# Kernel optimization log

Measured on AMD Instinct MI355X. Metric: run time of the kernel, lower is better.

Reference implementation:

```python
import jax, jax.numpy as jnp
import numpy as np

B, C, P, H, W = 8, 256, 64, 64, 64


def conv2d(x, w, b, pad):
    y = jax.lax.conv_general_dilated(
        x, w, window_strides=(1, 1), padding=[(pad, pad), (pad, pad)],
        dimension_numbers=("NCHW", "OIHW", "NCHW"))
    return y + b[None, :, None, None]


def setup_inputs() -> dict:
    key = jax.random.key(0)
    ks = jax.random.split(key, 9)
    x = jax.random.normal(ks[0], (B, C, H, W), dtype=jnp.float32)
    # conv weights, OIHW layout; scale ~ kaiming-ish
    w_top = jax.random.normal(ks[1], (P, C, 1, 1), jnp.float32) * (1.0 / np.sqrt(C))
    b_top = jnp.zeros((P,), jnp.float32)
    w_center = jax.random.normal(ks[2], (P, C, 1, 1), jnp.float32) * (1.0 / np.sqrt(C))
    b_center = jnp.zeros((P,), jnp.float32)
    w_bottom = jax.random.normal(ks[3], (C, C, 3, 3), jnp.float32) * (1.0 / np.sqrt(9 * C))
    b_bottom = jnp.zeros((C,), jnp.float32)
    w_out = jax.random.normal(ks[4], (C, C, 3, 3), jnp.float32) * (1.0 / np.sqrt(9 * C))
    b_out = jnp.zeros((C,), jnp.float32)
    return {"x": x, "w_top": w_top, "b_top": b_top, "w_center": w_center,
            "b_center": b_center, "w_bottom": w_bottom, "b_bottom": b_bottom,
            "w_out": w_out, "b_out": b_out}


def reference(x, w_top, b_top, w_center, b_center, w_bottom, b_bottom, w_out, b_out):
    b, c, h, w = x.shape
    hw = h * w
    x_top = conv2d(x, w_top, b_top, 0).reshape(b, -1, hw)          # [B, P, HW]
    x_center = conv2d(x, w_center, b_center, 0).reshape(b, -1, hw)  # [B, P, HW]
    x_center = jnp.swapaxes(x_center, 1, 2)                          # [B, HW, P]
    x_bottom = conv2d(x, w_bottom, b_bottom, 1).reshape(b, c, hw)
    x_bottom = jnp.swapaxes(x_bottom, 1, 2)                          # [B, HW, C]
    sp_map = jnp.einsum("bnp,bpm->bnm", x_center, x_top)            # [B, HW, HW]
    # NOTE: softmax is GLOBAL over the flattened HW*HW map per batch element,
    # not per-row (faithful to original Softmax(dim=1) on view(bsize, -1)).
    sp_map = jax.nn.softmax(sp_map.reshape(b, -1), axis=1).reshape(b, hw, hw)
    sp_map = jnp.einsum("bnm,bmc->bnc", sp_map, x_bottom)           # [B, HW, C]
    # NOTE: original does .reshape(b, C, h, w) on a [B, HW, C] tensor (no
    # transpose) -- replicate that exact memory reinterpretation.
    sp_map = sp_map.reshape(b, c, h, w)
    return conv2d(x + sp_map, w_out, b_out, 1)
```

## Files before the change

### kernel.cpp

```cpp
#include <hip/hip_runtime.h>
#include <hip/hip_bf16.h>
#include <type_traits>

constexpr int B_ = 8, C_ = 256, P_ = 64, H_ = 64, W_ = 64, HW_ = 4096;

typedef __attribute__((ext_vector_type(8))) short short8;
typedef __attribute__((ext_vector_type(4))) short short4v;
typedef __attribute__((ext_vector_type(4))) float f32x4;

__device__ __forceinline__ short bfbits(float f) {
    __hip_bfloat16 h = __float2bfloat16(f);
    return *reinterpret_cast<short*>(&h);
}
__device__ __forceinline__ float bf2f(short s) {
    __hip_bfloat16 h = *reinterpret_cast<__hip_bfloat16*>(&s);
    return (float)h;
}

#define GLL16(gsrc, ldst)                                                      \
    __builtin_amdgcn_global_load_lds(                                         \
        (const __attribute__((address_space(1))) void*)(gsrc),                \
        (__attribute__((address_space(3))) void*)(ldst), 16, 0, 0)


__global__ __launch_bounds__(256) void k_prep_w(
    const float* __restrict__ w, short8* __restrict__ wbP)
{
    const int idx = blockIdx.x * 256 + threadIdx.x;
    const int lane = idx & 63, cot = (idx >> 6) & 15;
    const int cb = (idx >> 10) & 7, tap = idx >> 13;
    const int lm = lane & 15, lq = lane >> 4;
    const int co = cot * 16 + lm, ci0 = cb * 32 + lq * 8;
    short8 v;
#pragma unroll
    for (int k = 0; k < 8; ++k)
        v[k] = bfbits(w[(co * 256 + ci0 + k) * 9 + tap]);
    wbP[idx] = v;
}

__global__ __launch_bounds__(256) void k_pack_xb(
    const __hip_bfloat16* __restrict__ xb, short8* __restrict__ xbP)
{
    const int tid = blockIdx.x * 256 + threadIdx.x;
    const int lane = tid & 63, wid = tid >> 6;
    const int ct = wid & 15, g = (wid >> 4) & 127, b = wid >> 11;
    const int c = ct * 16 + (lane >> 2);
    const int mo = g * 32 + (lane & 3) * 8;
    const short8 v = *reinterpret_cast<const short8*>(
        &xb[((size_t)(b * 256 + c)) * HW_ + mo]);
    xbP[(size_t)wid * 64 + (lane & 3) * 16 + (lane >> 2)] = v;
}

__global__ __launch_bounds__(256) void k_conv1x1(
    const float* __restrict__ x,
    const float* __restrict__ w_top, const float* __restrict__ b_top,
    const float* __restrict__ w_cen, const float* __restrict__ b_cen,
    short8* __restrict__ xtPh, short8* __restrict__ xtPl,
    short8* __restrict__ xcPh, short8* __restrict__ xcPl)
{
    const int b = blockIdx.z;
    const int n = blockIdx.x * 256 + threadIdx.x;
    const int conv = blockIdx.y >> 2, pq = blockIdx.y & 3;
    const int p0 = pq * 16;
    const float* w    = conv ? w_cen : w_top;
    const float* bias = conv ? b_cen : b_top;
    short8* oh = conv ? xcPh : xtPh;
    short8* ol = conv ? xcPl : xtPl;

    const float* xp = x + (size_t)b * C_ * HW_ + n;
    float acc[16];
#pragma unroll
    for (int p = 0; p < 16; ++p) acc[p] = 0.f;

    for (int c = 0; c < C_; c += 4) {
        const float xv0 = xp[(size_t)(c + 0) * HW_];
        const float xv1 = xp[(size_t)(c + 1) * HW_];
        const float xv2 = xp[(size_t)(c + 2) * HW_];
        const float xv3 = xp[(size_t)(c + 3) * HW_];
#pragma unroll
        for (int p = 0; p < 16; ++p) {
            const float4 wv = *reinterpret_cast<const float4*>(&w[(p0 + p) * C_ + c]);
            float a = acc[p];
            a = fmaf(wv.x, xv0, a);
            a = fmaf(wv.y, xv1, a);
            a = fmaf(wv.z, xv2, a);
            a = fmaf(wv.w, xv3, a);
            acc[p] = a;
        }
    }
    const int nt = n >> 4, lmn = n & 15;
    const size_t obase = ((size_t)(b * 256 + nt) * 2 + (pq >> 1)) * 64 + lmn;
#pragma unroll
    for (int jj = 0; jj < 2; ++jj) {
        short8 vh, vl;
#pragma unroll
        for (int k = 0; k < 8; ++k) {
            const float v = acc[jj * 8 + k] + bias[p0 + jj * 8 + k];
            const short hb = bfbits(v);
            vh[k] = hb;
            vl[k] = bfbits(v - bf2f(hb));
        }
        const size_t idx = obase + (size_t)(((pq & 1) * 2 + jj) * 16);
        oh[idx] = vh;
        ol[idx] = vl;
    }
}

template <typename OT>
__global__ __launch_bounds__(512, 4) void k_conv3x3_mfma(
    const float* __restrict__ xin, const short8* __restrict__ wbP,
    const float* __restrict__ bias, OT* __restrict__ out)
{
    __shared__ __align__(16) __hip_bfloat16 Xs[3][66][40];
    const int lin = blockIdx.x;
    const int b = lin & 7, h = lin >> 3;
    const int t = threadIdx.x;
    const int wave = t >> 6, lane = t & 63;
    const int lm = lane & 15, lq = lane >> 4;
    const int cobase = wave * 32;
    const int cot0 = wave * 2;

    f32x4 acc[4][2];
#pragma unroll
    for (int i = 0; i < 4; ++i)
#pragma unroll
        for (int j = 0; j < 2; ++j) acc[i][j] = f32x4{0.f, 0.f, 0.f, 0.f};

    if (t < 192) {
        const int r = t >> 6, cc = t & 31, side = (t >> 5) & 1;
        Xs[r][side ? 65 : 0][cc] = __float2bfloat16(0.f);
    }

    const float* xbase = xin + (size_t)b * C_ * HW_;

    for (int cb = 0; cb < 8; ++cb) {
        const int ci0 = cb * 32;
        __syncthreads();
#pragma unroll
        for (int it = 0; it < 3; ++it) {
            const int idx = it * 512 + t;
            const int r = idx >> 9, ci = (idx >> 4) & 31, wq = idx & 15;
            const int hh = h + r - 1;
            float4 v = {0.f, 0.f, 0.f, 0.f};
            if (hh >= 0 && hh < H_)
                v = *reinterpret_cast<const float4*>(
                    &xbase[(size_t)(ci0 + ci) * HW_ + hh * W_ + wq * 4]);
            Xs[r][1 + wq * 4 + 0][ci] = __float2bfloat16(v.x);
            Xs[r][1 + wq * 4 + 1][ci] = __float2bfloat16(v.y);
            Xs[r][1 + wq * 4 + 2][ci] = __float2bfloat16(v.z);
            Xs[r][1 + wq * 4 + 3][ci] = __float2bfloat16(v.w);
        }
        __syncthreads();

#pragma unroll 3
        for (int tap = 0; tap < 9; ++tap) {
            const int dh = tap / 3;
            const int dw = tap % 3;
            const short8* wp = wbP + ((size_t)(tap * 8 + cb)) * 1024 + lane;
            short8 af[2];
            af[0] = wp[(cot0 + 0) * 64];
            af[1] = wp[(cot0 + 1) * 64];
            short8 bf[4];
#pragma unroll
            for (int nt = 0; nt < 4; ++nt)
                bf[nt] = *reinterpret_cast<const short8*>(
                    &Xs[dh][nt * 16 + lm + dw][lq * 8]);
#pragma unroll
            for (int nt = 0; nt < 4; ++nt)
#pragma unroll
                for (int ct = 0; ct < 2; ++ct)
                    acc[nt][ct] = __builtin_amdgcn_mfma_f32_16x16x32_bf16(
                        af[ct], bf[nt], acc[nt][ct], 0, 0, 0);
        }
    }

#pragma unroll
    for (int nt = 0; nt < 4; ++nt) {
        const int pos = h * W_ + nt * 16 + lm;
#pragma unroll
        for (int ct = 0; ct < 2; ++ct) {
            const int co = cobase + ct * 16 + lq * 4;
#pragma unroll
            for (int r = 0; r < 4; ++r) {
                const float v = acc[nt][ct][r] + bias[co + r];
                if constexpr (std::is_same<OT, __hip_bfloat16>::value)
                    out[((size_t)(b * C_ + co + r)) * HW_ + pos] = __float2bfloat16(v);
                else
                    out[((size_t)(b * C_ + co + r)) * HW_ + pos] = v;
            }
        }
    }
}

__global__ __launch_bounds__(512, 2) void k_attn_mfma(
    const short8* __restrict__ xtPh, const short8* __restrict__ xtPl,
    const short8* __restrict__ xcPh, const short8* __restrict__ xcPl,
    const short8* __restrict__ xbP, float* __restrict__ O,
    float* __restrict__ Z)
{
    extern __shared__ __align__(16) char smem[];
    short8* XTs = (short8*)smem;
    short8* XBs = (short8*)(smem + 32768);
    short8* Ps8 = (short8*)(smem + 98304);
    short4v* Ps4 = (short4v*)(smem + 98304);
    float* zred = (float*)(smem + 114688);

    const int lin = blockIdx.x;
    const int b = lin & 7, nblk = lin >> 3;
    const int n0 = nblk * 128;

    const int t = threadIdx.x, wv = t >> 6, lane = t & 63;
    const int lm = lane & 15, lq = lane >> 4;
    const int mh = wv >> 2, nq2 = wv & 3;
    const int nq = wv >> 2, cq = wv & 3;

    short8 cB2[2][2][2];
#pragma unroll
    for (int ntile = 0; ntile < 2; ++ntile) {
        const int gt = nblk * 8 + nq2 * 2 + ntile;
        const size_t base = ((size_t)(b * 256 + gt) * 2) * 64 + lane;
        cB2[ntile][0][0] = xcPh[base];
        cB2[ntile][1][0] = xcPh[base + 64];
        cB2[ntile][0][1] = xcPl[base];
        cB2[ntile][1][1] = xcPl[base + 64];
    }
    asm volatile("s_waitcnt vmcnt(0)" ::: "memory");

    auto stage = [&](int smt, int bufi) {
        short8* XT = XTs + bufi * 1024;
        short8* XB = XBs + bufi * 2048;
        const size_t abase = ((size_t)(b * 512 + smt * 8)) * 64;
#pragma unroll
        for (int k = 0; k < 2; ++k) {
            const int c = wv * 2 + k, ms = c >> 2, part = c & 3;
            const short8* src = (part < 2 ? xtPh : xtPl)
                                + abase + ms * 128 + (part & 1) * 64 + lane;
            GLL16(src, XT + c * 64);
        }
        const size_t p8 = ((size_t)(b * 2048 + smt * 32)) * 64;
#pragma unroll
        for (int k = 0; k < 4; ++k) {
            const int e = k * 512 + wv * 64;
            GLL16(xbP + p8 + e + lane, XB + e);
        }
    };
    stage(0, 0);

    f32x4 acc[4][4];
#pragma unroll
    for (int i = 0; i < 4; ++i)
#pragma unroll
        for (int jj = 0; jj < 4; ++jj) acc[i][jj] = f32x4{0.f, 0.f, 0.f, 0.f};
    float zp = 0.f;

    for (int mt = 0; mt < 64; ++mt) {
        const int cur = mt & 1;
        asm volatile("s_waitcnt vmcnt(4)" ::: "memory");
        __builtin_amdgcn_sched_barrier(0);
        __builtin_amdgcn_s_barrier();
        __builtin_amdgcn_sched_barrier(0);
        stage((mt + 1) & 63, cur ^ 1);

        const short8* XT = XTs + cur * 1024;
#pragma unroll
        for (int ms2 = 0; ms2 < 2; ++ms2) {
            const int ms = mh * 2 + ms2;
            const short8 aH0 = XT[(ms * 4 + 0) * 64 + lane];
            const short8 aH1 = XT[(ms * 4 + 1) * 64 + lane];
            const short8 aL0 = XT[(ms * 4 + 2) * 64 + lane];
            const short8 aL1 = XT[(ms * 4 + 3) * 64 + lane];
#pragma unroll
            for (int ntile = 0; ntile < 2; ++ntile) {
                f32x4 s = {0.f, 0.f, 0.f, 0.f};
                __builtin_amdgcn_s_setprio(1);
                s = __builtin_amdgcn_mfma_f32_16x16x32_bf16(aH0, cB2[ntile][0][0], s, 0, 0, 0);
                s = __builtin_amdgcn_mfma_f32_16x16x32_bf16(aH1, cB2[ntile][1][0], s, 0, 0, 0);
                s = __builtin_amdgcn_mfma_f32_16x16x32_bf16(aH0, cB2[ntile][0][1], s, 0, 0, 0);
                s = __builtin_amdgcn_mfma_f32_16x16x32_bf16(aH1, cB2[ntile][1][1], s, 0, 0, 0);
                s = __builtin_amdgcn_mfma_f32_16x16x32_bf16(aL0, cB2[ntile][0][0], s, 0, 0, 0);
                s = __builtin_amdgcn_mfma_f32_16x16x32_bf16(aL1, cB2[ntile][1][0], s, 0, 0, 0);
                __builtin_amdgcn_s_setprio(0);
                const float e0 = __expf(s[0]), e1 = __expf(s[1]);
                const float e2 = __expf(s[2]), e3 = __expf(s[3]);
                zp += (e0 + e1) + (e2 + e3);
                short4v pk = { bfbits(e0), bfbits(e1), bfbits(e2), bfbits(e3) };
                const int T = nq2 * 2 + ntile;
                const int lqp = (ms & 1) * 2 + (lq >> 1);
                Ps4[(((T * 2 + mh) * 64) + lqp * 16 + lm) * 2 + (lq & 1)] = pk;
            }
        }
        asm volatile("s_waitcnt vmcnt(6) lgkmcnt(0)" ::: "memory");
        __builtin_amdgcn_sched_barrier(0);
        __builtin_amdgcn_s_barrier();
        __builtin_amdgcn_sched_barrier(0);

        const short8* XB = XBs + cur * 2048;
        short8 vb0[4], vb1[4];
#pragma unroll
        for (int q4 = 0; q4 < 4; ++q4) {
            const int ct = cq * 4 + q4;
            vb0[q4] = XB[ct * 64 + lane];
            vb1[q4] = XB[1024 + ct * 64 + lane];
        }
#pragma unroll
        for (int nt2 = 0; nt2 < 4; ++nt2) {
            const int T = nq * 4 + nt2;
            const short8 pa0 = Ps8[(T * 2 + 0) * 64 + lane];
            const short8 pa1 = Ps8[(T * 2 + 1) * 64 + lane];
            __builtin_amdgcn_s_setprio(1);
#pragma unroll
            for (int q4 = 0; q4 < 4; ++q4) {
                acc[nt2][q4] = __builtin_amdgcn_mfma_f32_16x16x32_bf16(
                    pa0, vb0[q4], acc[nt2][q4], 0, 0, 0);
                acc[nt2][q4] = __builtin_amdgcn_mfma_f32_16x16x32_bf16(
                    pa1, vb1[q4], acc[nt2][q4], 0, 0, 0);
            }
            __builtin_amdgcn_s_setprio(0);
        }
    }

#pragma unroll
    for (int o = 32; o > 0; o >>= 1) zp += __shfl_down(zp, o, 64);
    if (lane == 0) zred[wv] = zp;
    __syncthreads();
    if (t == 0) {
        float zs = 0.f;
#pragma unroll
        for (int wvi = 0; wvi < 8; ++wvi) zs += zred[wvi];
        atomicAdd(&Z[b], zs);
    }

#pragma unroll
    for (int nt2 = 0; nt2 < 4; ++nt2) {
#pragma unroll
        for (int q4 = 0; q4 < 4; ++q4) {
            const int c = cq * 64 + q4 * 16 + lm;
#pragma unroll
            for (int r = 0; r < 4; ++r) {
                const int n = n0 + (nq * 4 + nt2) * 16 + lq * 4 + r;
                O[((size_t)b * HW_ + n) * C_ + c] = acc[nt2][q4][r];
            }
        }
    }
}

__global__ __launch_bounds__(256) void k_add(
    const float* __restrict__ x, const float* __restrict__ o,
    const float* __restrict__ Z, float* __restrict__ y)
{
    const int bidx = blockIdx.x;
    const float invZ = 1.0f / Z[bidx >> 10];
    const size_t i = ((size_t)bidx * 256 + threadIdx.x) * 4;
    const float4 a = *reinterpret_cast<const float4*>(&x[i]);
    const float4 b = *reinterpret_cast<const float4*>(&o[i]);
    float4 r{fmaf(b.x, invZ, a.x), fmaf(b.y, invZ, a.y),
             fmaf(b.z, invZ, a.z), fmaf(b.w, invZ, a.w)};
    *reinterpret_cast<float4*>(&y[i]) = r;
}

extern "C" void kernel_launch(void* const* d_in, const int* in_sizes, int n_in,
                              void* d_out, int out_size, void* d_ws, size_t ws_size,
                              hipStream_t stream)
{
    const float* x   = (const float*)d_in[0];
    const float* wt  = (const float*)d_in[1];
    const float* bt  = (const float*)d_in[2];
    const float* wc  = (const float*)d_in[3];
    const float* bc  = (const float*)d_in[4];
    const float* wbo = (const float*)d_in[5];
    const float* bbo = (const float*)d_in[6];
    const float* wo  = (const float*)d_in[7];
    const float* bo  = (const float*)d_in[8];
    float* out = (float*)d_out;

    uint8_t* w8 = (uint8_t*)d_ws;
    const size_t MB = 1u << 20;
    short8* xtPh = (short8*)(w8);
    short8* xtPl = (short8*)(w8 + 4 * MB);
    short8* xcPh = (short8*)(w8 + 8 * MB);
    short8* xcPl = (short8*)(w8 + 12 * MB);
    __hip_bfloat16* xbB = (__hip_bfloat16*)(w8 + 16 * MB);
    short8* xbP  = (short8*)(w8 + 32 * MB);
    float*  O    = (float*)(w8 + 48 * MB);
    short8* Wb1  = (short8*)(w8 + 48 * MB);
    short8* Wb2  = (short8*)(w8 + 32 * MB);
    float*  y    = (float*)(w8);
    float*  Z    = (float*)(w8 + 80 * MB);

    hipMemsetAsync(Z, 0, B_ * sizeof(float), stream);
    k_prep_w<<<dim3(288), 256, 0, stream>>>(wbo, Wb1);
    k_conv1x1<<<dim3(16, 8, 8), 256, 0, stream>>>(x, wt, bt, wc, bc,
                                                  xtPh, xtPl, xcPh, xcPl);
    k_conv3x3_mfma<__hip_bfloat16><<<dim3(512), 512, 0, stream>>>(x, Wb1, bbo, xbB);
    k_pack_xb<<<dim3(4096), 256, 0, stream>>>(xbB, xbP);
    k_attn_mfma<<<dim3(256), dim3(512), 114720, stream>>>(xtPh, xtPl, xcPh, xcPl,
                                                          xbP, O, Z);
    k_prep_w<<<dim3(288), 256, 0, stream>>>(wo, Wb2);
    k_add<<<dim3(8192), 256, 0, stream>>>(x, O, Z, y);
    k_conv3x3_mfma<float><<<dim3(512), 512, 0, stream>>>(y, Wb2, bo, out);
}
```

Before: 386.7 us.

## Pre-pack conv3x3 inputs to swizzled bf16 and double-buffer LDS via direct global loads

Adds pack kernels that convert the conv3x3 input (x, and x plus scaled attention output) into a padded, XOR-swizzled bf16 layout, fusing the residual add into the second pack. The conv3x3 kernel then stages 64-channel blocks straight into LDS with global_load_lds, double-buffered so the next block loads while the current one computes. The swizzle is meant to avoid LDS bank conflicts. This removes the per-block fp32 load, convert and scatter inside the conv and halves the number of barriers. In exchange it adds two extra passes over the input and uses more LDS, which may lower occupancy.

```diff
diff --git a/kernel.cpp b/kernel.cpp
--- a/kernel.cpp
+++ b/kernel.cpp
@@ -51,6 +51,65 @@
     xbP[(size_t)wid * 64 + (lane & 3) * 16 + (lane >> 2)] = v;
 }
 
+__global__ __launch_bounds__(256) void k_pack_x(
+    const float* __restrict__ src, short8* __restrict__ dst)
+{
+    const int tid = blockIdx.x * 256 + threadIdx.x;
+    const int lane = tid & 63, wid = tid >> 6;
+    const int hs = wid % 66, cbk = (wid / 66) & 3, b = wid / 264;
+    const int hh = hs - 1;
+    short8 v[8];
+    if (hh < 0 || hh > 63) {
+#pragma unroll
+        for (int s = 0; s < 8; ++s)
+            v[s] = short8{0, 0, 0, 0, 0, 0, 0, 0};
+    } else {
+        const float* sp = src + (size_t)b * C_ * HW_ + hh * 64 + lane;
+#pragma unroll
+        for (int s = 0; s < 8; ++s) {
+            const int g = s ^ ((lane + 1) & 7);
+#pragma unroll
+            for (int j = 0; j < 8; ++j)
+                v[s][j] = bfbits(sp[(size_t)(cbk * 64 + g * 8 + j) * HW_]);
+        }
+    }
+    short8* dp = dst + (size_t)wid * 512 + lane * 8;
+#pragma unroll
+    for (int s = 0; s < 8; ++s) dp[s] = v[s];
+}
+
+__global__ __launch_bounds__(256) void k_add_pack(
+    const float* __restrict__ x, const float* __restrict__ O,
+    const float* __restrict__ Z, short8* __restrict__ dst)
+{
+    const int tid = blockIdx.x * 256 + threadIdx.x;
+    const int lane = tid & 63, wid = tid >> 6;
+    const int hs = wid % 66, cbk = (wid / 66) & 3, b = wid / 264;
+    const int hh = hs - 1;
+    short8 v[8];
+    if (hh < 0 || hh > 63) {
+#pragma unroll
+        for (int s = 0; s < 8; ++s)
+            v[s] = short8{0, 0, 0, 0, 0, 0, 0, 0};
+    } else {
+        const float invZ = 1.0f / Z[b];
+        const float* xp = x + (size_t)b * C_ * HW_ + hh * 64 + lane;
+        const float* op = O + (size_t)b * HW_ * C_ + hh * 64 + lane;
+#pragma unroll
+        for (int s = 0; s < 8; ++s) {
+            const int g = s ^ ((lane + 1) & 7);
+#pragma unroll
+            for (int j = 0; j < 8; ++j) {
+                const size_t off = (size_t)(cbk * 64 + g * 8 + j) * HW_;
+                v[s][j] = bfbits(fmaf(op[off], invZ, xp[off]));
+            }
+        }
+    }
+    short8* dp = dst + (size_t)wid * 512 + lane * 8;
+#pragma unroll
+    for (int s = 0; s < 8; ++s) dp[s] = v[s];
+}
+
 __global__ __launch_bounds__(256) void k_conv1x1(
     const float* __restrict__ x,
     const float* __restrict__ w_top, const float* __restrict__ b_top,
@@ -108,10 +167,10 @@
 
 template <typename OT>
 __global__ __launch_bounds__(512, 4) void k_conv3x3_mfma(
-    const float* __restrict__ xin, const short8* __restrict__ wbP,
+    const short8* __restrict__ xPk, const short8* __restrict__ wbP,
     const float* __restrict__ bias, OT* __restrict__ out)
 {
-    __shared__ __align__(16) __hip_bfloat16 Xs[3][66][40];
+    __shared__ __align__(16) char Xs[2][3][66 * 128];
     const int lin = blockIdx.x;
     const int b = lin & 7, h = lin >> 3;
     const int t = threadIdx.x;
@@ -120,57 +179,71 @@
     const int cobase = wave * 32;
     const int cot0 = wave * 2;
 
+    if (t < 384) {
+        const int bufi = t / 192, rem = t % 192;
+        const int rs = rem / 32, col = rem % 32;
+        const int tl = rs >> 1, row = (rs & 1) ? 65 : 0;
+        *reinterpret_cast<int*>(&Xs[bufi][tl][row * 128 + col * 4]) = 0;
+    }
+
+    auto stage = [&](int cbk, int bufi) {
+#pragma unroll
+        for (int j = 0; j < 3; ++j) {
+            const int q = wave * 3 + j;
+            const int r = q >> 3, c = q & 7;
+            const short8* src = xPk +
+                ((size_t)((b * 4 + cbk) * 66 + h + r) * 512 + c * 64 + lane);
+            GLL16(src, &Xs[bufi][r][128 + c * 1024]);
+        }
+    };
+
     f32x4 acc[4][2];
 #pragma unroll
     for (int i = 0; i < 4; ++i)
 #pragma unroll
         for (int j = 0; j < 2; ++j) acc[i][j] = f32x4{0.f, 0.f, 0.f, 0.f};
 
-    if (t < 192) {
-        const int r = t >> 6, cc = t & 31, side = (t >> 5) & 1;
-        Xs[r][side ? 65 : 0][cc] = __float2bfloat16(0.f);
-    }
-
-    const float* xbase = xin + (size_t)b * C_ * HW_;
-
-    for (int cb = 0; cb < 8; ++cb) {
-        const int ci0 = cb * 32;
-        __syncthreads();
-#pragma unroll
-        for (int it = 0; it < 3; ++it) {
-            const int idx = it * 512 + t;
-            const int r = idx >> 9, ci = (idx >> 4) & 31, wq = idx & 15;
-            const int hh = h + r - 1;
-            float4 v = {0.f, 0.f, 0.f, 0.f};
-            if (hh >= 0 && hh < H_)
-                v = *reinterpret_cast<const float4*>(
-                    &xbase[(size_t)(ci0 + ci) * HW_ + hh * W_ + wq * 4]);
-            Xs[r][1 + wq * 4 + 0][ci] = __float2bfloat16(v.x);
-            Xs[r][1 + wq * 4 + 1][ci] = __float2bfloat16(v.y);
-            Xs[r][1 + wq * 4 + 2][ci] = __float2bfloat16(v.z);
-            Xs[r][1 + wq * 4 + 3][ci] = __float2bfloat16(v.w);
-        }
-        __syncthreads();
+    __syncthreads();
+    stage(0, 0);
+
+    for (int cbk = 0; cbk < 4; ++cbk) {
+        const int cur = cbk & 1;
+        asm volatile("s_waitcnt vmcnt(0)" ::: "memory");
+        __builtin_amdgcn_sched_barrier(0);
+        __builtin_amdgcn_s_barrier();
+        __builtin_amdgcn_sched_barrier(0);
+        if (cbk < 3) stage(cbk + 1, cur ^ 1);
 
 #pragma unroll 3
         for (int tap = 0; tap < 9; ++tap) {
             const int dh = tap / 3;
             const int dw = tap % 3;
-            const short8* wp = wbP + ((size_t)(tap * 8 + cb)) * 1024 + lane;
-            short8 af[2];
-            af[0] = wp[(cot0 + 0) * 64];
-            af[1] = wp[(cot0 + 1) * 64];
-            short8 bf[4];
+            const short8* wp = wbP + ((size_t)(tap * 8 + cbk * 2)) * 1024 + lane;
+            short8 af[2][2];
+            af[0][0] = wp[(cot0 + 0) * 64];
+            af[0][1] = wp[(cot0 + 1) * 64];
+            af[1][0] = wp[1024 + (cot0 + 0) * 64];
+            af[1][1] = wp[1024 + (cot0 + 1) * 64];
+            short8 bf[4][2];
+#pragma unroll
+            for (int nt = 0; nt < 4; ++nt) {
+                const int row = nt * 16 + lm + dw;
+#pragma unroll
+                for (int kc = 0; kc < 2; ++kc) {
+                    const int s = (kc * 4 + lq) ^ (row & 7);
+                    bf[nt][kc] = *reinterpret_cast<const short8*>(
+                        &Xs[cur][dh][row * 128 + s * 16]);
+                }
+            }
 #pragma unroll
             for (int nt = 0; nt < 4; ++nt)
-                bf[nt] = *reinterpret_cast<const short8*>(
-                    &Xs[dh][nt * 16 + lm + dw][lq * 8]);
-#pragma unroll
-            for (int nt = 0; nt < 4; ++nt)
-#pragma unroll
-                for (int ct = 0; ct < 2; ++ct)
+#pragma unroll
+                for (int ct = 0; ct < 2; ++ct) {
                     acc[nt][ct] = __builtin_amdgcn_mfma_f32_16x16x32_bf16(
-                        af[ct], bf[nt], acc[nt][ct], 0, 0, 0);
+                        af[0][ct], bf[nt][0], acc[nt][ct], 0, 0, 0);
+                    acc[nt][ct] = __builtin_amdgcn_mfma_f32_16x16x32_bf16(
+                        af[1][ct], bf[nt][1], acc[nt][ct], 0, 0, 0);
+                }
         }
     }
 
@@ -344,20 +417,6 @@
     }
 }
 
-__global__ __launch_bounds__(256) void k_add(
-    const float* __restrict__ x, const float* __restrict__ o,
-    const float* __restrict__ Z, float* __restrict__ y)
-{
-    const int bidx = blockIdx.x;
-    const float invZ = 1.0f / Z[bidx >> 10];
-    const size_t i = ((size_t)bidx * 256 + threadIdx.x) * 4;
-    const float4 a = *reinterpret_cast<const float4*>(&x[i]);
-    const float4 b = *reinterpret_cast<const float4*>(&o[i]);
-    float4 r{fmaf(b.x, invZ, a.x), fmaf(b.y, invZ, a.y),
-             fmaf(b.z, invZ, a.z), fmaf(b.w, invZ, a.w)};
-    *reinterpret_cast<float4*>(&y[i]) = r;
-}
-
 extern "C" void kernel_launch(void* const* d_in, const int* in_sizes, int n_in,
                               void* d_out, int out_size, void* d_ws, size_t ws_size,
                               hipStream_t stream)
@@ -380,22 +439,24 @@
     short8* xcPh = (short8*)(w8 + 8 * MB);
     short8* xcPl = (short8*)(w8 + 12 * MB);
     __hip_bfloat16* xbB = (__hip_bfloat16*)(w8 + 16 * MB);
+    short8* xPk  = (short8*)(w8 + 32 * MB);
     short8* xbP  = (short8*)(w8 + 32 * MB);
     float*  O    = (float*)(w8 + 48 * MB);
-    short8* Wb1  = (short8*)(w8 + 48 * MB);
+    short8* Wb1  = (short8*)(w8 + 56 * MB);
     short8* Wb2  = (short8*)(w8 + 32 * MB);
-    float*  y    = (float*)(w8);
+    short8* yPk  = (short8*)(w8);
     float*  Z    = (float*)(w8 + 80 * MB);
 
     hipMemsetAsync(Z, 0, B_ * sizeof(float), stream);
     k_prep_w<<<dim3(288), 256, 0, stream>>>(wbo, Wb1);
+    k_pack_x<<<dim3(528), 256, 0, stream>>>(x, xPk);
     k_conv1x1<<<dim3(16, 8, 8), 256, 0, stream>>>(x, wt, bt, wc, bc,
                                                   xtPh, xtPl, xcPh, xcPl);
-    k_conv3x3_mfma<__hip_bfloat16><<<dim3(512), 512, 0, stream>>>(x, Wb1, bbo, xbB);
+    k_conv3x3_mfma<__hip_bfloat16><<<dim3(512), 512, 0, stream>>>(xPk, Wb1, bbo, xbB);
     k_pack_xb<<<dim3(4096), 256, 0, stream>>>(xbB, xbP);
     k_attn_mfma<<<dim3(256), dim3(512), 114720, stream>>>(xtPh, xtPl, xcPh, xcPl,
                                                           xbP, O, Z);
     k_prep_w<<<dim3(288), 256, 0, stream>>>(wo, Wb2);
-    k_add<<<dim3(8192), 256, 0, stream>>>(x, O, Z, y);
-    k_conv3x3_mfma<float><<<dim3(512), 512, 0, stream>>>(y, Wb2, bo, out);
-}
+    k_add_pack<<<dim3(528), 256, 0, stream>>>(x, O, Z, yPk);
+    k_conv3x3_mfma<float><<<dim3(512), 512, 0, stream>>>(yPk, Wb2, bo, out);
+}
```

Measured after the change: 473.0 us. +22.3%, slower.
